# Optimization experiments

Measured on AMD Instinct MI355X. Metric: run time of the kernel, lower is better.

The kernel has to match this reference:

```python
import jax, jax.numpy as jnp
import numpy as np

NUM_CLASSES = 3
W_CE, W_DICE, W_LOVASZ, W_BOUNDARY, W_TOPO = 0.4, 0.3, 0.2, 0.08, 0.02
DICE_SMOOTH = 1e-5
LOVASZ_SUBSAMPLE_THRESH = 100000
LOVASZ_SUBSAMPLE_N = 50000


def _lovasz_hinge_flat(logits, fg):
    # logits, fg: [N]; fg in {0,1}. Sort errors descending, Lovasz gradient, dot.
    signs = 2.0 * fg - 1.0
    errors = 1.0 - logits * signs
    order = jnp.argsort(-errors)          # descending (stable)
    errors_sorted = errors[order]
    gt_sorted = fg[order]
    gts = gt_sorted.sum()
    intersection = gts - jnp.cumsum(gt_sorted)
    union = gts + jnp.cumsum(1.0 - gt_sorted)
    jaccard = 1.0 - intersection / jnp.maximum(union, 1e-12)
    jaccard = jnp.concatenate([jaccard[:1], jaccard[1:] - jaccard[:-1]])
    grad = jnp.where(gts > 0, jaccard, jnp.zeros_like(jaccard))  # gts==0 -> zero grad
    return jnp.dot(jax.nn.relu(errors_sorted), grad)


def structural_loss(predictions, labels):
    B, C, H, W = predictions.shape
    log_probs = jax.nn.log_softmax(predictions, axis=1)      # [B,C,H,W]
    probs = jnp.exp(log_probs)
    # ---- Cross entropy (mean) and per-pixel CE (reused by boundary loss) ----
    ce_pix = -jnp.take_along_axis(log_probs, labels[:, None, :, :], axis=1)[:, 0]  # [B,H,W]
    ce = ce_pix.mean()
    # ---- Dice loss (flattened over whole batch, per class) ----
    one_hot = jax.nn.one_hot(labels, C, dtype=probs.dtype, axis=1)  # [B,C,H,W]
    inter = jnp.sum(probs * one_hot, axis=(0, 2, 3))                 # [C]
    denom = jnp.sum(probs, axis=(0, 2, 3)) + jnp.sum(one_hot, axis=(0, 2, 3))
    dice_scores = (2.0 * inter + DICE_SMOOTH) / (denom + DICE_SMOOTH)
    dice = 1.0 - dice_scores.mean()
    # ---- Lovasz-Softmax ('present' classes, flat over batch, subsampled) ----
    p_flat = probs.transpose(0, 2, 3, 1).reshape(-1, C)  # [N,C]
    l_flat = labels.reshape(-1)                          # [N]
    N = l_flat.shape[0]
    lov_key = jax.random.key(42)
    losses, weights = [], []
    for c in range(C):
        fg_full = (l_flat == c).astype(probs.dtype)
        present = (fg_full.sum() > 0).astype(probs.dtype)
        logits_full = fg_full - p_flat[:, c]
        if N > LOVASZ_SUBSAMPLE_THRESH:
            idx = jax.random.permutation(jax.random.fold_in(lov_key, c), N)[:LOVASZ_SUBSAMPLE_N]
            logits_c, fg_c = logits_full[idx], fg_full[idx]
        else:
            logits_c, fg_c = logits_full, fg_full
        losses.append(_lovasz_hinge_flat(logits_c, fg_c))
        weights.append(present)
    losses = jnp.stack(losses)
    wts = jnp.stack(weights)
    lovasz = jnp.sum(losses * wts) / jnp.maximum(jnp.sum(wts), 1.0)
    # ---- Boundary loss: np.gradient-style boundary mask on classes {1,2} ----
    bnd = jnp.zeros(labels.shape, dtype=bool)
    for c in (1, 2):
        cm = (labels == c).astype(jnp.float32)          # [B,H,W]
        gx = jnp.abs(jnp.gradient(cm, axis=2))
        gy = jnp.abs(jnp.gradient(cm, axis=1))
        bnd = bnd | ((gx + gy) > 0.1)
    bmask = bnd.astype(predictions.dtype)
    boundary = jnp.sum(ce_pix * bmask) / (jnp.sum(bmask) + 1e-8)
    # ---- Topology loss (component count degenerates to presence indicator) ----
    topo = jnp.asarray(0.0, dtype=predictions.dtype)
    for c in (1, 2):
        gt_comp = jnp.any(labels == c, axis=(1, 2)).astype(predictions.dtype)      # [B]
        pred_comp = jnp.any(probs[:, c] > 0.5, axis=(1, 2)).astype(predictions.dtype)
        topo = topo + jnp.sum(jnp.maximum(pred_comp - gt_comp, 0.0) ** 2)
    topo = topo / B
    return (W_CE * ce + W_DICE * dice + W_LOVASZ * lovasz
            + W_BOUNDARY * boundary + W_TOPO * topo)


def setup_inputs() -> dict:
    key = jax.random.key(0)
    k1, k2 = jax.random.split(key)
    predictions = jax.random.normal(k1, (16, 3, 1024, 1024), dtype=jnp.float32)
    labels = jax.random.randint(k2, (16, 1024, 1024), 0, 3)
    return {"predictions": predictions, "labels": labels}


def reference(predictions, labels):
    return structural_loss(predictions, labels)
```

## Files before the change

kernel.cpp:

```cpp
#include <hip/hip_runtime.h>
#include <cstdint>
#include <cstddef>

#define K_BINS 256
#define NBLK   2048
#define TPB    256
#define ROWS_PER_BLK 8
#define HW_    1048576u
#define W_     1024u
#define NPIX   16777216u
#define NHIST  (3*K_BINS)
#define NBLK_S (NBLK/8)

#define PA_OFF   0
#define PU_OFF   32768
#define PL_OFF   49152
#define FH_OFF   65536
#define PART_OFF 81920

#define GLD_LDS(SRC, DST)                                                      \
    __builtin_amdgcn_global_load_lds(                                          \
        (const __attribute__((address_space(1))) void*)(SRC),                  \
        (__attribute__((address_space(3))) void*)(DST), 16, 0, 0)

__device__ __forceinline__ void hist_add(unsigned int* h, int c, float e, int isfg) {
    int bin = (int)(e * (float)K_BINS);
    bin = bin < 0 ? 0 : (bin > K_BINS - 1 ? K_BINS - 1 : bin);
    atomicAdd(&h[c * K_BINS + bin], isfg ? 1u : 65536u);
}

__global__ __launch_bounds__(TPB, 3) void k_main(
    const float* __restrict__ pred, const int* __restrict__ lab,
    double* __restrict__ pa, unsigned long long* __restrict__ pu,
    unsigned long long* __restrict__ pl,
    unsigned int* __restrict__ finalhist, unsigned int* __restrict__ part, int use_dump)
{
    __shared__ float spbuf[4][3][1024];
    __shared__ unsigned int h[NHIST];
    __shared__ float redf[2][TPB / 64];
    __shared__ unsigned int redu[TPB / 64];
    __shared__ unsigned long long redl[TPB / 64];

    const int wv   = threadIdx.x >> 6;
    const int lane = threadIdx.x & 63;
    const bool do_hist = ((blockIdx.x & 7u) == 0u);

    const unsigned gr0   = blockIdx.x * ROWS_PER_BLK;
    const unsigned batch = gr0 >> 10;
    const unsigned i0    = gr0 & 1023u;
    const unsigned col   = threadIdx.x * 4u;
    const int*   labimg  = lab  + (size_t)batch * HW_;
    const float* predimg = pred + (size_t)(batch * 3u) * HW_;
    const unsigned bsh = batch * 4u;

#define STAGE(TR)                                                              \
    {                                                                          \
        const unsigned gi = i0 + (unsigned)(TR);                               \
        _Pragma("unroll")                                                      \
        for (int s_ = 0; s_ < 3; ++s_) {                                       \
            const int k_ = wv * 3 + s_;                                        \
            const int c_ = k_ >> 2, q_ = k_ & 3;                               \
            const float* src_ = predimg + (size_t)c_ * HW_ + (size_t)gi * W_   \
                              + (unsigned)(q_ * 256 + lane * 4);               \
            GLD_LDS(src_, &spbuf[(TR) & 3][c_][q_ * 256]);                     \
        }                                                                      \
    }

#define LROW(RR) (labimg + (size_t)((RR) < 0 ? 0 : ((RR) > 1023 ? 1023 : (RR))) * W_)

    if (do_hist) {
        for (int idx = threadIdx.x; idx < NHIST; idx += TPB) h[idx] = 0u;
    }

    const int ii0 = (int)i0;
    const bool has_lf = (col > 0u), has_rt = (col < 1020u);

    int4 lprev = *(const int4*)(LROW(ii0 - 1) + col);
    int4 lcur  = *(const int4*)(LROW(ii0)     + col);
    int4 ln0   = *(const int4*)(LROW(ii0 + 1) + col);
    int lf0 = has_lf ? LROW(ii0)[col - 1u] : 0;
    int rt0 = has_rt ? LROW(ii0)[col + 4u] : 0;
    STAGE(0)
    asm volatile("" ::: "memory");
    int4 ln1 = *(const int4*)(LROW(ii0 + 2) + col);
    int lf1 = has_lf ? LROW(ii0 + 1)[col - 1u] : 0;
    int rt1 = has_rt ? LROW(ii0 + 1)[col + 4u] : 0;
    STAGE(1)
    asm volatile("" ::: "memory");

    float ce_acc = 0.f, bce_acc = 0.f;
    unsigned bcnt = 0;
    unsigned long long fl = 0ull;
    int4 ln2; int lf2, rt2;

#define PIXEL(A0, A1, A2, L, BND)                                              \
        {                                                                      \
            const float a0 = (A0), a1 = (A1), a2 = (A2); const int l = (L);    \
            const float m  = fmaxf(fmaxf(a0, a1), a2);                         \
            const float e0 = __expf(a0 - m), e1 = __expf(a1 - m), e2 = __expf(a2 - m); \
            const float s  = e0 + e1 + e2;                                     \
            const float lse = m + __logf(s);                                   \
            const float al = (l == 0) ? a0 : ((l == 1) ? a1 : a2);             \
            const float ce = lse - al;                                         \
            const float inv = __builtin_amdgcn_rcpf(s);                        \
            const float p0 = e0 * inv, p1 = e1 * inv, p2 = e2 * inv;           \
            ce_acc += ce;                                                      \
            if (BND) { bce_acc += ce; bcnt++; }                                \
            unsigned mbit = (l == 1 ? 1u : 0u) | (l == 2 ? 2u : 0u) |          \
                            (p1 > 0.5f ? 4u : 0u) | (p2 > 0.5f ? 8u : 0u);     \
            fl |= ((unsigned long long)mbit) << bsh;                           \
            if (do_hist) {                                                     \
                hist_add(h, 0, (l == 0) ? p0 : (1.0f - p0), l == 0);           \
                hist_add(h, 1, (l == 1) ? p1 : (1.0f - p1), l == 1);           \
                hist_add(h, 2, (l == 2) ? p2 : (1.0f - p2), l == 2);           \
            }                                                                  \
        }

#define COMPUTE(R)                                                             \
    {                                                                          \
        const float* b0p = spbuf[(R) & 3][0];                                  \
        const float* b1p = spbuf[(R) & 3][1];                                  \
        const float* b2p = spbuf[(R) & 3][2];                                  \
        const float4 C0 = *(const float4*)(b0p + col);                         \
        const float4 C1 = *(const float4*)(b1p + col);                         \
        const float4 C2 = *(const float4*)(b2p + col);                         \
        const int hd0 = (col == 0u)    ? (lcur.x != lcur.y) : (lf0 != lcur.y); \
        const int hd1 = (lcur.x != lcur.z);                                    \
        const int hd2 = (lcur.y != lcur.w);                                    \
        const int hd3 = (col == 1020u) ? (lcur.z != lcur.w) : (lcur.z != rt0); \
        const int vd0 = (lprev.x != ln0.x), vd1 = (lprev.y != ln0.y);          \
        const int vd2 = (lprev.z != ln0.z), vd3 = (lprev.w != ln0.w);          \
        PIXEL(C0.x, C1.x, C2.x, lcur.x, (hd0 | vd0))                           \
        PIXEL(C0.y, C1.y, C2.y, lcur.y, (hd1 | vd1))                           \
        PIXEL(C0.z, C1.z, C2.z, lcur.z, (hd2 | vd2))                           \
        PIXEL(C0.w, C1.w, C2.w, lcur.w, (hd3 | vd3))                           \
    }                                                                          \
    lprev = lcur; lcur = ln0; ln0 = ln1; ln1 = ln2;                            \
    lf0 = lf1; rt0 = rt1; lf1 = lf2; rt1 = rt2;

    STAGE(2)
    ln2 = *(const int4*)(LROW(ii0 + 3) + col);
    lf2 = has_lf ? LROW(ii0 + 2)[col - 1u] : 0;
    rt2 = has_rt ? LROW(ii0 + 2)[col + 4u] : 0;
    asm volatile("s_waitcnt vmcnt(12) lgkmcnt(0)" ::: "memory");
    __builtin_amdgcn_s_barrier();
    COMPUTE(0)

    for (int r = 1; r <= ROWS_PER_BLK - 3; ++r) {
        STAGE(r + 2)
        ln2 = *(const int4*)(LROW(ii0 + r + 3) + col);
        lf2 = has_lf ? LROW(ii0 + r + 2)[col - 1u] : 0;
        rt2 = has_rt ? LROW(ii0 + r + 2)[col + 4u] : 0;
        asm volatile("s_waitcnt vmcnt(12)" ::: "memory");
        __builtin_amdgcn_s_barrier();
        COMPUTE(r)
    }

    asm volatile("s_waitcnt vmcnt(6)" ::: "memory");
    __builtin_amdgcn_s_barrier();
    COMPUTE(ROWS_PER_BLK - 2)

    asm volatile("s_waitcnt vmcnt(0)" ::: "memory");
    __builtin_amdgcn_s_barrier();
    COMPUTE(ROWS_PER_BLK - 1)

#undef PIXEL
#undef COMPUTE
#undef STAGE
#undef LROW

#pragma unroll
    for (int off = 32; off; off >>= 1) {
        ce_acc  += __shfl_down(ce_acc, off);
        bce_acc += __shfl_down(bce_acc, off);
        bcnt    += __shfl_down(bcnt, off);
        fl      |= __shfl_down(fl, off);
    }
    if ((threadIdx.x & 63) == 0) {
        redf[0][wv] = ce_acc; redf[1][wv] = bce_acc;
        redu[wv] = bcnt;
        redl[wv] = fl;
    }
    __syncthreads();
    if (threadIdx.x == 0) {
        double a0 = 0, a1 = 0; unsigned int u = 0; unsigned long long L = 0ull;
        for (int w2 = 0; w2 < TPB / 64; w2++) {
            a0 += (double)redf[0][w2]; a1 += (double)redf[1][w2];
            u += redu[w2]; L |= redl[w2];
        }
        pa[blockIdx.x * 2 + 0] = a0;
        pa[blockIdx.x * 2 + 1] = a1;
        pu[blockIdx.x] = (unsigned long long)u;
        pl[blockIdx.x] = L;
    }

    if (do_hist) {
        __syncthreads();
        if (use_dump) {
            unsigned int* dst = part + (size_t)(blockIdx.x >> 3) * NHIST;
            for (int idx = threadIdx.x; idx < NHIST; idx += TPB) dst[idx] = h[idx];
        } else {
            for (int idx = threadIdx.x; idx < NHIST; idx += TPB) {
                unsigned int v = h[idx];
                if (v & 0xFFFFu)  atomicAdd(&finalhist[idx * 2 + 0], v & 0xFFFFu);
                if (v >> 16)      atomicAdd(&finalhist[idx * 2 + 1], v >> 16);
            }
        }
    }
}

__global__ __launch_bounds__(256) void k_reduce(const unsigned int* __restrict__ part,
                                               unsigned int* __restrict__ finalhist)
{
    const int f = blockIdx.x * 256 + threadIdx.x;
    unsigned int lo = 0, hi = 0;
    for (int blk = 0; blk < NBLK_S; ++blk) {
        const unsigned int v = part[(size_t)blk * NHIST + f];
        lo += v & 0xFFFFu;
        hi += v >> 16;
    }
    finalhist[f * 2 + 0] = lo;
    finalhist[f * 2 + 1] = hi;
}

__global__ __launch_bounds__(1024) void k_final(
    const double* __restrict__ pa, const unsigned long long* __restrict__ pu,
    const unsigned long long* __restrict__ pl,
    const unsigned int* __restrict__ finalhist, float* __restrict__ out)
{
    __shared__ unsigned int sf[K_BINS], sb[K_BINS];
    __shared__ double red[16];
    __shared__ double red4[16][4];
    __shared__ double lres[3];
    __shared__ double dInter[3], dSumP[3], dCnt[3];
    __shared__ double tot[3];
    __shared__ unsigned long long totL;
    const int t = threadIdx.x;

    {
        double a0 = pa[t * 2 + 0] + pa[(t + 1024) * 2 + 0];
        double a1 = pa[t * 2 + 1] + pa[(t + 1024) * 2 + 1];
        double uu = (double)pu[t] + (double)pu[t + 1024];
        unsigned long long L = pl[t] | pl[t + 1024];
#pragma unroll
        for (int off = 32; off; off >>= 1) {
            a0 += __shfl_down(a0, off);
            a1 += __shfl_down(a1, off);
            uu += __shfl_down(uu, off);
            L  |= __shfl_down(L, off);
        }
        if ((t & 63) == 0) { red4[t >> 6][0] = a0; red4[t >> 6][1] = a1;
                             red4[t >> 6][2] = uu;
                             red[t >> 6] = __longlong_as_double((long long)L); }
        __syncthreads();
        if (t == 0) {
            double s0 = 0, s1 = 0, s2 = 0; unsigned long long LL = 0ull;
            for (int w2 = 0; w2 < 16; ++w2) {
                s0 += red4[w2][0]; s1 += red4[w2][1]; s2 += red4[w2][2];
                LL |= (unsigned long long)__double_as_longlong(red[w2]);
            }
            tot[0] = s0; tot[1] = s1; tot[2] = s2; totL = LL;
        }
        __syncthreads();
    }

    for (int c = 0; c < 3; ++c) {
        unsigned int fgc = 0, bgc = 0;
        if (t < K_BINS) {
            fgc = finalhist[(c * K_BINS + t) * 2 + 0];
            bgc = finalhist[(c * K_BINS + t) * 2 + 1];
            sf[t] = fgc; sb[t] = bgc;
        }
        const double ec = ((double)t + 0.5) / (double)K_BINS;
        double s0 = (t < K_BINS) ? (double)fgc : 0.0;
        double s1 = (t < K_BINS) ? (double)fgc * ec : 0.0;
        double s2 = (t < K_BINS) ? (double)bgc : 0.0;
        double s3 = (t < K_BINS) ? (double)bgc * ec : 0.0;
#pragma unroll
        for (int off = 32; off; off >>= 1) {
            s0 += __shfl_down(s0, off); s1 += __shfl_down(s1, off);
            s2 += __shfl_down(s2, off); s3 += __shfl_down(s3, off);
        }
        if ((t & 63) == 0) { red4[t >> 6][0] = s0; red4[t >> 6][1] = s1;
                             red4[t >> 6][2] = s2; red4[t >> 6][3] = s3; }
        __syncthreads();
        if (t == 0) {
            double cntf = 0, sfe = 0, cntb = 0, sbe = 0;
            for (int w2 = 0; w2 < 16; ++w2) {
                cntf += red4[w2][0]; sfe += red4[w2][1];
                cntb += red4[w2][2]; sbe += red4[w2][3];
            }
            const double inter = sfe;
            dInter[c] = inter;
            dSumP[c]  = inter + (cntb - sbe);
            dCnt[c]   = cntf;
        }
        __syncthreads();

        for (int off = 1; off < K_BINS; off <<= 1) {
            unsigned int vf = 0, vb = 0;
            if (t < K_BINS) {
                vf = sf[t] + ((t + off < K_BINS) ? sf[t + off] : 0u);
                vb = sb[t] + ((t + off < K_BINS) ? sb[t + off] : 0u);
            }
            __syncthreads();
            if (t < K_BINS) { sf[t] = vf; sb[t] = vb; }
            __syncthreads();
        }
        const unsigned int gtsu = sf[0];
        double Jk = 0.0;
        if (t >= 1 && t < K_BINS && gtsu > 0u) {
            const double gts = (double)gtsu;
            Jk = 1.0 - (gts - (double)sf[t]) / (gts + (double)sb[t]);
        }
#pragma unroll
        for (int off = 32; off; off >>= 1) Jk += __shfl_down(Jk, off);
        if ((t & 63) == 0) red[t >> 6] = Jk;
        __syncthreads();
        if (t == 0) {
            double sj = 0; for (int w2 = 0; w2 < 16; ++w2) sj += red[w2];
            lres[c] = (gtsu > 0u) ? ((0.5 + sj) / (double)K_BINS) : -1.0;
        }
        __syncthreads();
    }

    if (t == 0) {
        const double N = 16777216.0;
        const double ce = tot[0] / N;
        double dsum = 0.0;
        for (int c = 0; c < 3; c++) {
            dsum += (2.0 * dInter[c] + 1e-5) / (dSumP[c] + dCnt[c] + 1e-5);
        }
        const double dice = 1.0 - dsum / 3.0;
        double lsum = 0.0, wsum = 0.0;
        for (int c = 0; c < 3; c++) {
            if (lres[c] >= 0.0) { lsum += lres[c]; wsum += 1.0; }
        }
        const double lovasz = lsum / fmax(wsum, 1.0);
        const double bnd = tot[1] / (tot[2] + 1e-8);
        const unsigned long long fl = totL;
        double topo = 0.0;
        for (int b = 0; b < 16; b++) {
            for (int c2 = 0; c2 < 2; c2++) {
                const double gt = (double)((fl >> (b * 4 + c2)) & 1ull);
                const double pr = (double)((fl >> (b * 4 + 2 + c2)) & 1ull);
                const double d = pr - gt;
                if (d > 0.0) topo += d * d;
            }
        }
        topo /= 16.0;
        out[0] = (float)(0.4 * ce + 0.3 * dice + 0.2 * lovasz + 0.08 * bnd + 0.02 * topo);
    }
}

extern "C" void kernel_launch(void* const* d_in, const int* in_sizes, int n_in,
                              void* d_out, int out_size, void* d_ws, size_t ws_size,
                              hipStream_t stream)
{
    const float* pred = (const float*)d_in[0];
    const int*   lab  = (const int*)d_in[1];
    float* out = (float*)d_out;

    char* wsb = (char*)d_ws;
    double* pa = (double*)(wsb + PA_OFF);
    unsigned long long* pu = (unsigned long long*)(wsb + PU_OFF);
    unsigned long long* pl = (unsigned long long*)(wsb + PL_OFF);
    unsigned int* finalhist = (unsigned int*)(wsb + FH_OFF);
    unsigned int* part = (unsigned int*)(wsb + PART_OFF);
    const size_t need = (size_t)PART_OFF + (size_t)NBLK_S * NHIST * 4u;
    const int use_dump = (ws_size >= need) ? 1 : 0;

    if (!use_dump)
        hipMemsetAsync(finalhist, 0, NHIST * 2 * sizeof(unsigned int), stream);

    hipLaunchKernelGGL(k_main, dim3(NBLK), dim3(TPB), 0, stream,
                       pred, lab, pa, pu, pl, finalhist, part, use_dump);
    if (use_dump)
        hipLaunchKernelGGL(k_reduce, dim3(NHIST / 256), dim3(256), 0, stream, part, finalhist);
    hipLaunchKernelGGL(k_final, dim3(1), dim3(1024), 0, stream, pa, pu, pl, finalhist, out);
}
```

Baseline: 86.15 us.

## Make pixel staging wave-private to drop barriers and parallelize histogram reduction

Each wave now stages only its own 256-column slice of all three channels into LDS through global_load_lds. Because no wave reads another wave's staged data, the per-row s_barriers can go, and waves advance independently on vmcnt waits alone. The histogram zeroing moves ahead of a single __syncthreads. The partial-histogram reduction is split from 3 blocks of long serial loops into 24 blocks, and k_final sums the 8 resulting partials. This shortens the serial latency chain of the reduce kernel, at the cost of a little extra work and workspace in the final kernel.

```diff
diff --git a/kernel.cpp b/kernel.cpp
--- a/kernel.cpp
+++ b/kernel.cpp
@@ -11,12 +11,14 @@
 #define NPIX   16777216u
 #define NHIST  (3*K_BINS)
 #define NBLK_S (NBLK/8)
-
-#define PA_OFF   0
-#define PU_OFF   32768
-#define PL_OFF   49152
-#define FH_OFF   65536
-#define PART_OFF 81920
+#define NRED_I 8
+
+#define PA_OFF    0
+#define PU_OFF    32768
+#define PL_OFF    49152
+#define FH_OFF    65536
+#define PART_OFF  81920
+#define PART2_OFF 868352
 
 #define GLD_LDS(SRC, DST)                                                      \
     __builtin_amdgcn_global_load_lds(                                          \
@@ -53,24 +55,23 @@
     const float* predimg = pred + (size_t)(batch * 3u) * HW_;
     const unsigned bsh = batch * 4u;
 
+    if (do_hist) {
+        for (int idx = threadIdx.x; idx < NHIST; idx += TPB) h[idx] = 0u;
+    }
+    __syncthreads();
+
 #define STAGE(TR)                                                              \
     {                                                                          \
         const unsigned gi = i0 + (unsigned)(TR);                               \
         _Pragma("unroll")                                                      \
-        for (int s_ = 0; s_ < 3; ++s_) {                                       \
-            const int k_ = wv * 3 + s_;                                        \
-            const int c_ = k_ >> 2, q_ = k_ & 3;                               \
+        for (int c_ = 0; c_ < 3; ++c_) {                                       \
             const float* src_ = predimg + (size_t)c_ * HW_ + (size_t)gi * W_   \
-                              + (unsigned)(q_ * 256 + lane * 4);               \
-            GLD_LDS(src_, &spbuf[(TR) & 3][c_][q_ * 256]);                     \
+                              + (unsigned)(wv * 256 + lane * 4);               \
+            GLD_LDS(src_, &spbuf[(TR) & 3][c_][wv * 256]);                     \
         }                                                                      \
     }
 
 #define LROW(RR) (labimg + (size_t)((RR) < 0 ? 0 : ((RR) > 1023 ? 1023 : (RR))) * W_)
-
-    if (do_hist) {
-        for (int idx = threadIdx.x; idx < NHIST; idx += TPB) h[idx] = 0u;
-    }
 
     const int ii0 = (int)i0;
     const bool has_lf = (col > 0u), has_rt = (col < 1020u);
@@ -142,8 +143,7 @@
     ln2 = *(const int4*)(LROW(ii0 + 3) + col);
     lf2 = has_lf ? LROW(ii0 + 2)[col - 1u] : 0;
     rt2 = has_rt ? LROW(ii0 + 2)[col + 4u] : 0;
-    asm volatile("s_waitcnt vmcnt(12) lgkmcnt(0)" ::: "memory");
-    __builtin_amdgcn_s_barrier();
+    asm volatile("s_waitcnt vmcnt(12)" ::: "memory");
     COMPUTE(0)
 
     for (int r = 1; r <= ROWS_PER_BLK - 3; ++r) {
@@ -152,16 +152,13 @@
         lf2 = has_lf ? LROW(ii0 + r + 2)[col - 1u] : 0;
         rt2 = has_rt ? LROW(ii0 + r + 2)[col + 4u] : 0;
         asm volatile("s_waitcnt vmcnt(12)" ::: "memory");
-        __builtin_amdgcn_s_barrier();
         COMPUTE(r)
     }
 
     asm volatile("s_waitcnt vmcnt(6)" ::: "memory");
-    __builtin_amdgcn_s_barrier();
     COMPUTE(ROWS_PER_BLK - 2)
 
     asm volatile("s_waitcnt vmcnt(0)" ::: "memory");
-    __builtin_amdgcn_s_barrier();
     COMPUTE(ROWS_PER_BLK - 1)
 
 #undef PIXEL
@@ -195,7 +192,6 @@
     }
 
     if (do_hist) {
-        __syncthreads();
         if (use_dump) {
             unsigned int* dst = part + (size_t)(blockIdx.x >> 3) * NHIST;
             for (int idx = threadIdx.x; idx < NHIST; idx += TPB) dst[idx] = h[idx];
@@ -210,23 +206,27 @@
 }
 
 __global__ __launch_bounds__(256) void k_reduce(const unsigned int* __restrict__ part,
-                                               unsigned int* __restrict__ finalhist)
+                                               unsigned int* __restrict__ part2)
 {
-    const int f = blockIdx.x * 256 + threadIdx.x;
+    const int och = blockIdx.x % 3;
+    const int ich = blockIdx.x / 3;
+    const int f = och * 256 + threadIdx.x;
     unsigned int lo = 0, hi = 0;
-    for (int blk = 0; blk < NBLK_S; ++blk) {
+    const int b0 = ich * (NBLK_S / NRED_I);
+    for (int blk = b0; blk < b0 + NBLK_S / NRED_I; ++blk) {
         const unsigned int v = part[(size_t)blk * NHIST + f];
         lo += v & 0xFFFFu;
         hi += v >> 16;
     }
-    finalhist[f * 2 + 0] = lo;
-    finalhist[f * 2 + 1] = hi;
+    part2[((size_t)ich * NHIST + f) * 2 + 0] = lo;
+    part2[((size_t)ich * NHIST + f) * 2 + 1] = hi;
 }
 
 __global__ __launch_bounds__(1024) void k_final(
     const double* __restrict__ pa, const unsigned long long* __restrict__ pu,
     const unsigned long long* __restrict__ pl,
-    const unsigned int* __restrict__ finalhist, float* __restrict__ out)
+    const unsigned int* __restrict__ part2, const unsigned int* __restrict__ finalhist,
+    int use_dump, float* __restrict__ out)
 {
     __shared__ unsigned int sf[K_BINS], sb[K_BINS];
     __shared__ double red[16];
@@ -267,8 +267,16 @@
     for (int c = 0; c < 3; ++c) {
         unsigned int fgc = 0, bgc = 0;
         if (t < K_BINS) {
-            fgc = finalhist[(c * K_BINS + t) * 2 + 0];
-            bgc = finalhist[(c * K_BINS + t) * 2 + 1];
+            if (use_dump) {
+#pragma unroll
+                for (int i = 0; i < NRED_I; ++i) {
+                    fgc += part2[((size_t)i * NHIST + c * K_BINS + t) * 2 + 0];
+                    bgc += part2[((size_t)i * NHIST + c * K_BINS + t) * 2 + 1];
+                }
+            } else {
+                fgc = finalhist[(c * K_BINS + t) * 2 + 0];
+                bgc = finalhist[(c * K_BINS + t) * 2 + 1];
+            }
             sf[t] = fgc; sb[t] = bgc;
         }
         const double ec = ((double)t + 0.5) / (double)K_BINS;
@@ -367,7 +375,8 @@
     unsigned long long* pl = (unsigned long long*)(wsb + PL_OFF);
     unsigned int* finalhist = (unsigned int*)(wsb + FH_OFF);
     unsigned int* part = (unsigned int*)(wsb + PART_OFF);
-    const size_t need = (size_t)PART_OFF + (size_t)NBLK_S * NHIST * 4u;
+    unsigned int* part2 = (unsigned int*)(wsb + PART2_OFF);
+    const size_t need = (size_t)PART2_OFF + (size_t)NRED_I * NHIST * 2u * 4u;
     const int use_dump = (ws_size >= need) ? 1 : 0;
 
     if (!use_dump)
@@ -376,6 +385,7 @@
     hipLaunchKernelGGL(k_main, dim3(NBLK), dim3(TPB), 0, stream,
                        pred, lab, pa, pu, pl, finalhist, part, use_dump);
     if (use_dump)
-        hipLaunchKernelGGL(k_reduce, dim3(NHIST / 256), dim3(256), 0, stream, part, finalhist);
-    hipLaunchKernelGGL(k_final, dim3(1), dim3(1024), 0, stream, pa, pu, pl, finalhist, out);
-}
+        hipLaunchKernelGGL(k_reduce, dim3(24), dim3(256), 0, stream, part, part2);
+    hipLaunchKernelGGL(k_final, dim3(1), dim3(1024), 0, stream,
+                       pa, pu, pl, part2, finalhist, use_dump, out);
+}
```

Result: faster. 76.79 us (-10.9%).
